# Optimization experiments

Hardware: AMD Instinct MI355X
Metric: run time of the kernel (lower is better)

The kernel has to match this reference:

```python
import jax, jax.numpy as jnp
import numpy as np

B, IN, H, G, WR = 8192, 1024, 1024, 2, 64
UR = [64, 64]


def setup_inputs() -> dict:
    key = jax.random.key(0)
    ks = jax.random.split(key, 9)
    hg = H // G
    return {
        "x": jax.random.normal(ks[0], (B, IN), jnp.float32),
        "h": jax.random.normal(ks[1], (B, H), jnp.float32),
        "c": jax.random.normal(ks[2], (B, H), jnp.float32),
        "u_x": 0.1 * jax.random.normal(ks[3], (IN, WR), jnp.float32),
        "v_x": 0.1 * jax.random.normal(ks[4], (4 * H, WR), jnp.float32),
        "u_h_0": 0.1 * jax.random.normal(ks[5], (G, hg, UR[0]), jnp.float32),
        "v_h_0": 0.1 * jax.random.normal(ks[6], (G, UR[0], 4 * hg), jnp.float32),
        "u_h_1": 0.1 * jax.random.normal(ks[7], (G, hg, UR[1]), jnp.float32),
        "v_h_1": 0.1 * jax.random.normal(ks[8], (G, UR[1], 4 * hg), jnp.float32),
        "bias_x": jnp.ones((1, 4 * H), jnp.float32),
        "bias_h": jnp.ones((1, 4 * H), jnp.float32),
    }


def reference(x, h, c, u_x, v_x, u_h_0, v_h_0, u_h_1, v_h_1, bias_x, bias_h):
    b = h.shape[0]
    hg = H // G
    # input-to-hidden low-rank projection: [B, 4H]
    gx = (x @ u_x) @ v_x.T + bias_x
    xf, xi, xn, xo = jnp.split(gx, 4, axis=1)  # each [B, H]

    hv = h.reshape(b, G, hg)  # [B, G, H/G]
    u_hs = [u_h_0, u_h_1]
    v_hs = [v_h_0, v_h_1]
    acc = None
    for i in range(G):
        # torch code rotates the group index list cumulatively each step:
        # step i uses permutation roll(arange(G), -i)
        perm = np.roll(np.arange(G), -i)
        h_op = hv[:, perm, :]  # [B, G, hg]
        t = jnp.einsum('bgd,gdr->bgr', h_op, u_hs[i])  # [B, G, r_i]
        t = jnp.einsum('bgr,grk->bgk', t, v_hs[i])     # [B, G, 4hg]
        acc = t if acc is None else acc + t

    # chunk along last dim into 4 gates, flatten group dim -> [B, H]
    f_h, i_h, n_h, o_h = [p.reshape(b, H) for p in jnp.split(acc, 4, axis=2)]
    hf, hi, hn, ho = jnp.split(bias_h, 4, axis=1)

    inputgate = jax.nn.sigmoid(xi + hi + i_h)
    forgetgate = jax.nn.sigmoid(xf + hf + f_h)
    outputgate = jax.nn.sigmoid(xo + ho + o_h)
    newgate = jnp.tanh(xn + hn + n_h)
    c_next = forgetgate * c + inputgate * newgate
    h_next = outputgate * jnp.tanh(c_next)
    return (h_next, c_next)
```

## Files before the change

kernel.cpp:

```cpp
#include <hip/hip_runtime.h>
#include <hip/hip_bf16.h>


typedef __bf16 bf16_t;
typedef __bf16 bf16x8 __attribute__((ext_vector_type(8)));
typedef float f32x4 __attribute__((ext_vector_type(4)));

#define MFMA16x16x32(a, b, c) __builtin_amdgcn_mfma_f32_16x16x32_bf16((a), (b), (c), 0, 0, 0)

#define T_OFF 0
#define UXT_OFF 5242880
#define UHT_OFF 5373952
#define WB_OFF 5636096

__global__ __launch_bounds__(256) void prep_kernel(
    const float* __restrict__ u_x, const float* __restrict__ u_h_0,
    const float* __restrict__ u_h_1, const float* __restrict__ v_h_0,
    const float* __restrict__ v_h_1, const float* __restrict__ v_x,
    bf16_t* __restrict__ uxT, bf16_t* __restrict__ uhT,
    bf16_t* __restrict__ Wb) {
  int i = blockIdx.x * 256 + threadIdx.x;
  if (i < 65536) {
    int j = i >> 10, k = i & 1023;
    uxT[i] = (bf16_t)u_x[k * 64 + j];
  } else if (i < 65536 + 131072) {
    int i2 = i - 65536;
    int s = i2 >> 15, rem = i2 & 32767;
    int j = rem >> 9, d = rem & 511;
    const float* src = (s & 1) ? u_h_1 : u_h_0;
    int goff = (s >> 1) ? 32768 : 0;
    uhT[i2] = (bf16_t)src[goff + d * 64 + j];
  } else if (i < 65536 + 131072 + 786432) {
    int e = i - 196608;
    int k = e % 192;
    int row = e / 192;
    int tile = row >> 7;
    int rr = row & 127;
    int g = tile >> 4, qt = tile & 15;
    int w = rr >> 5, ql = rr & 31;
    int m = g * 512 + qt * 32 + ql;
    int q = qt * 32 + ql;
    float val;
    if (k < 64)
      val = v_x[(w * 1024 + m) * 64 + k];
    else if (k < 128)
      val = v_h_0[g * 131072 + (k - 64) * 2048 + w * 512 + q];
    else
      val = v_h_1[g * 131072 + (k - 128) * 2048 + w * 512 + q];
    Wb[e] = (bf16_t)val;
  }
}

__global__ __launch_bounds__(256, 2) void phase1_kernel(
    const float* __restrict__ x, const float* __restrict__ h,
    const bf16_t* __restrict__ uxT, const bf16_t* __restrict__ uhT,
    bf16_t* __restrict__ T) {
  __shared__ bf16_t z[16][1048];
  const int b0 = blockIdx.x * 16;
  const int tid = threadIdx.x;
  const int wv = tid >> 6, lane = tid & 63;
  const int lo = lane & 15, quad = lane >> 4;
  const int srow = tid >> 4, sc = tid & 15;

  {
    const float* src = x + (size_t)(b0 + srow) * 1024;
#pragma unroll
    for (int j = 0; j < 16; ++j) {
      int col = sc * 4 + j * 64;
      float4 v = *(const float4*)(src + col);
      bf16_t* d = &z[srow][col];
      d[0] = (bf16_t)v.x; d[1] = (bf16_t)v.y;
      d[2] = (bf16_t)v.z; d[3] = (bf16_t)v.w;
    }
  }
  __syncthreads();

  f32x4 accx = {0.f, 0.f, 0.f, 0.f};
  {
    const bf16_t* wBase = uxT + (size_t)(16 * wv + lo) * 1024;
    for (int k = 0; k < 1024; k += 32) {
      bf16x8 af = *(const bf16x8*)&z[lo][k + quad * 8];
      bf16x8 bfr = *(const bf16x8*)(wBase + k + quad * 8);
      accx = MFMA16x16x32(af, bfr, accx);
    }
  }
#pragma unroll
  for (int r = 0; r < 4; ++r)
    T[(size_t)(b0 + quad * 4 + r) * 320 + 16 * wv + lo] = (bf16_t)accx[r];
  __syncthreads();

  {
    const float* src = h + (size_t)(b0 + srow) * 1024;
#pragma unroll
    for (int j = 0; j < 16; ++j) {
      int col = sc * 4 + j * 64;
      float4 v = *(const float4*)(src + col);
      bf16_t* d = &z[srow][col];
      d[0] = (bf16_t)v.x; d[1] = (bf16_t)v.y;
      d[2] = (bf16_t)v.z; d[3] = (bf16_t)v.w;
    }
  }
  __syncthreads();

  const int hoff = (wv == 1 || wv == 2) ? 512 : 0;
#pragma unroll
  for (int sub = 0; sub < 4; ++sub) {
    const bf16_t* wBase = uhT + (size_t)(wv * 64 + 16 * sub + lo) * 512;
    f32x4 acc = {0.f, 0.f, 0.f, 0.f};
    for (int k = 0; k < 512; k += 32) {
      bf16x8 af = *(const bf16x8*)&z[lo][hoff + k + quad * 8];
      bf16x8 bfr = *(const bf16x8*)(wBase + k + quad * 8);
      acc = MFMA16x16x32(af, bfr, acc);
    }
    int n = 64 + wv * 64 + sub * 16 + lo;
#pragma unroll
    for (int r = 0; r < 4; ++r)
      T[(size_t)(b0 + quad * 4 + r) * 320 + n] = (bf16_t)acc[r];
  }
}

__global__ __launch_bounds__(256, 3) void phase2_kernel(
    const bf16_t* __restrict__ T, const bf16_t* __restrict__ Wb,
    const float* __restrict__ bias_x, const float* __restrict__ bias_h,
    const float* __restrict__ c, float* __restrict__ out) {
  __shared__ bf16_t bs[128][200];

  const int b0 = blockIdx.x * 128;
  const int gq = blockIdx.y;
  const int g = gq >> 4, qt = gq & 15;
  const int tid = threadIdx.x;
  const int wv = tid >> 6, lane = tid & 63;
  const int lo = lane & 15, quad = lane >> 4;

  {
    const bf16_t* src = Wb + (size_t)gq * (128 * 192);
#pragma unroll
    for (int cch = 0; cch < 12; ++cch) {
      int lc = cch * 256 + tid;
      int row = lc / 24, col = (lc % 24) * 8;
      bf16x8 v = *(const bf16x8*)(src + (size_t)lc * 8);
      *(bf16x8*)&bs[row][col] = v;
    }
  }

  const int arow = b0 + wv * 32 + lo;
  bf16x8 a[2][6];
#pragma unroll
  for (int mt = 0; mt < 2; ++mt) {
    const bf16_t* tr = T + (size_t)(arow + mt * 16) * 320;
#pragma unroll
    for (int ks = 0; ks < 6; ++ks) {
      int col = (ks < 2) ? (ks * 32 + quad * 8)
                         : (64 + g * 128 + (ks - 2) * 32 + quad * 8);
      a[mt][ks] = *(const bf16x8*)(tr + col);
    }
  }
  __syncthreads();

  f32x4 acc[2][8];
#pragma unroll
  for (int mt = 0; mt < 2; ++mt)
#pragma unroll
    for (int nt = 0; nt < 8; ++nt) acc[mt][nt] = (f32x4){0.f, 0.f, 0.f, 0.f};

#pragma unroll
  for (int nt = 0; nt < 8; ++nt) {
#pragma unroll
    for (int ks = 0; ks < 6; ++ks) {
      bf16x8 bfr = *(const bf16x8*)&bs[nt * 16 + lo][ks * 32 + quad * 8];
      acc[0][nt] = MFMA16x16x32(a[0][ks], bfr, acc[0][nt]);
      acc[1][nt] = MFMA16x16x32(a[1][ks], bfr, acc[1][nt]);
    }
  }

  float bsum[4][2];
#pragma unroll
  for (int w = 0; w < 4; ++w)
#pragma unroll
    for (int cq = 0; cq < 2; ++cq) {
      int m = g * 512 + qt * 32 + cq * 16 + lo;
      int n = w * 1024 + m;
      bsum[w][cq] = bias_x[n] + bias_h[n];
    }

#pragma unroll
  for (int mt = 0; mt < 2; ++mt)
#pragma unroll
    for (int r = 0; r < 4; ++r) {
      int b = b0 + wv * 32 + mt * 16 + quad * 4 + r;
#pragma unroll
      for (int cq = 0; cq < 2; ++cq) {
        int m = g * 512 + qt * 32 + cq * 16 + lo;
        float fv = acc[mt][0 + cq][r] + bsum[0][cq];
        float iv = acc[mt][2 + cq][r] + bsum[1][cq];
        float nv = acc[mt][4 + cq][r] + bsum[2][cq];
        float ov = acc[mt][6 + cq][r] + bsum[3][cq];
        float cin = c[(size_t)b * 1024 + m];
        float ig = 1.f / (1.f + __expf(-iv));
        float fg = 1.f / (1.f + __expf(-fv));
        float og = 1.f / (1.f + __expf(-ov));
        float ng = tanhf(nv);
        float cn = fg * cin + ig * ng;
        float hn = og * tanhf(cn);
        out[(size_t)b * 1024 + m] = hn;
        out[8388608ull + (size_t)b * 1024 + m] = cn;
      }
    }
}

extern "C" void kernel_launch(void* const* d_in, const int* in_sizes, int n_in,
                              void* d_out, int out_size, void* d_ws,
                              size_t ws_size, hipStream_t stream) {
  const float* x = (const float*)d_in[0];
  const float* h = (const float*)d_in[1];
  const float* c = (const float*)d_in[2];
  const float* u_x = (const float*)d_in[3];
  const float* v_x = (const float*)d_in[4];
  const float* u_h_0 = (const float*)d_in[5];
  const float* v_h_0 = (const float*)d_in[6];
  const float* u_h_1 = (const float*)d_in[7];
  const float* v_h_1 = (const float*)d_in[8];
  const float* bias_x = (const float*)d_in[9];
  const float* bias_h = (const float*)d_in[10];

  char* ws = (char*)d_ws;
  bf16_t* T = (bf16_t*)(ws + T_OFF);
  bf16_t* uxT = (bf16_t*)(ws + UXT_OFF);
  bf16_t* uhT = (bf16_t*)(ws + UHT_OFF);
  bf16_t* Wb = (bf16_t*)(ws + WB_OFF);

  prep_kernel<<<3840, 256, 0, stream>>>(u_x, u_h_0, u_h_1, v_h_0, v_h_1, v_x,
                                        uxT, uhT, Wb);
  phase1_kernel<<<512, 256, 0, stream>>>(x, h, uxT, uhT, T);
  phase2_kernel<<<dim3(64, 32), 256, 0, stream>>>(T, Wb, bias_x, bias_h, c,
                                                  (float*)d_out);
}
```

Baseline: 233.1 us.

## Store weights and intermediates in MFMA fragment-native layouts; drop phase2 LDS staging

Prep now writes the U and W weights pre-swizzled into per-lane MFMA fragment order. Phase1 stages its outputs in LDS and writes the intermediate T in the same fragment-tiled layout, so phase2 can load A and B fragments with contiguous 16-byte per-lane global reads. This removes phase2's shared-memory tile, its staging loop and its barrier. It also restructures the phase1 h loop to reuse the A fragment across four subtiles, packs the bf16 converts into vector stores, and swaps in rcp-based sigmoid and tanh. Phase2 now reads B fragments straight from global memory through the cache, and the fast tanh may lose a little accuracy.

Measured after the change: 205.9 us. 11.7% less time.

```diff
diff --git a/kernel.cpp b/kernel.cpp
--- a/kernel.cpp
+++ b/kernel.cpp
@@ -3,41 +3,55 @@
 
 
 typedef __bf16 bf16_t;
+typedef __bf16 bf16x4 __attribute__((ext_vector_type(4)));
 typedef __bf16 bf16x8 __attribute__((ext_vector_type(8)));
 typedef float f32x4 __attribute__((ext_vector_type(4)));
 
 #define MFMA16x16x32(a, b, c) __builtin_amdgcn_mfma_f32_16x16x32_bf16((a), (b), (c), 0, 0, 0)
 
-#define T_OFF 0
-#define UXT_OFF 5242880
-#define UHT_OFF 5373952
-#define WB_OFF 5636096
+#define TA_OFF 0
+#define BX_OFF 5242880
+#define BH_OFF 5373952
+#define BW_OFF 5636096
+
+__device__ inline float fast_sigmoid(float x) {
+  return __builtin_amdgcn_rcpf(1.f + __expf(-x));
+}
+__device__ inline float fast_tanh(float x) {
+  return 2.f * __builtin_amdgcn_rcpf(1.f + __expf(-2.f * x)) - 1.f;
+}
 
 __global__ __launch_bounds__(256) void prep_kernel(
     const float* __restrict__ u_x, const float* __restrict__ u_h_0,
     const float* __restrict__ u_h_1, const float* __restrict__ v_h_0,
     const float* __restrict__ v_h_1, const float* __restrict__ v_x,
-    bf16_t* __restrict__ uxT, bf16_t* __restrict__ uhT,
-    bf16_t* __restrict__ Wb) {
-  int i = blockIdx.x * 256 + threadIdx.x;
-  if (i < 65536) {
-    int j = i >> 10, k = i & 1023;
-    uxT[i] = (bf16_t)u_x[k * 64 + j];
-  } else if (i < 65536 + 131072) {
-    int i2 = i - 65536;
-    int s = i2 >> 15, rem = i2 & 32767;
-    int j = rem >> 9, d = rem & 511;
+    bf16_t* __restrict__ Bx, bf16_t* __restrict__ Bh,
+    bf16_t* __restrict__ Bw) {
+  int o = blockIdx.x * 256 + threadIdx.x;
+  if (o < 65536) {
+    int j = o & 7, lane = (o >> 3) & 63, kk = (o >> 9) & 31, t = o >> 14;
+    int lo = lane & 15, quad = lane >> 4;
+    int k = kk * 32 + quad * 8 + j;
+    Bx[o] = (bf16_t)u_x[k * 64 + 16 * t + lo];
+  } else if (o < 196608) {
+    int o2 = o - 65536;
+    int j = o2 & 7, lane = (o2 >> 3) & 63, kk = (o2 >> 9) & 15;
+    int sub = (o2 >> 13) & 3, s = o2 >> 15;
+    int lo = lane & 15, quad = lane >> 4;
+    int d = kk * 32 + quad * 8 + j;
     const float* src = (s & 1) ? u_h_1 : u_h_0;
-    int goff = (s >> 1) ? 32768 : 0;
-    uhT[i2] = (bf16_t)src[goff + d * 64 + j];
-  } else if (i < 65536 + 131072 + 786432) {
-    int e = i - 196608;
-    int k = e % 192;
-    int row = e / 192;
-    int tile = row >> 7;
-    int rr = row & 127;
-    int g = tile >> 4, qt = tile & 15;
-    int w = rr >> 5, ql = rr & 31;
+    Bh[o2] = (bf16_t)src[(s >> 1) * 32768 + d * 64 + 16 * sub + lo];
+  } else if (o < 983040) {
+    int o3 = o - 196608;
+    int j = o3 & 7, lane = (o3 >> 3) & 63;
+    int chunk = o3 >> 9;
+    int ks = chunk % 6, rowt = chunk / 6;
+    int gq = rowt >> 3, nt = rowt & 7;
+    int lo = lane & 15, quad = lane >> 4;
+    int g = gq >> 4, qt = gq & 15;
+    int row = 16 * nt + lo;
+    int w = row >> 5, ql = row & 31;
+    int k = ks * 32 + quad * 8 + j;
     int m = g * 512 + qt * 32 + ql;
     int q = qt * 32 + ql;
     float val;
@@ -47,15 +61,16 @@
       val = v_h_0[g * 131072 + (k - 64) * 2048 + w * 512 + q];
     else
       val = v_h_1[g * 131072 + (k - 128) * 2048 + w * 512 + q];
-    Wb[e] = (bf16_t)val;
-  }
-}
-
-__global__ __launch_bounds__(256, 2) void phase1_kernel(
+    Bw[o3] = (bf16_t)val;
+  }
+}
+
+__global__ __launch_bounds__(256) void phase1_kernel(
     const float* __restrict__ x, const float* __restrict__ h,
-    const bf16_t* __restrict__ uxT, const bf16_t* __restrict__ uhT,
-    bf16_t* __restrict__ T) {
+    const bf16_t* __restrict__ Bx, const bf16_t* __restrict__ Bh,
+    bf16_t* __restrict__ TA) {
   __shared__ bf16_t z[16][1048];
+  __shared__ bf16_t pre[16][328];
   const int b0 = blockIdx.x * 16;
   const int tid = threadIdx.x;
   const int wv = tid >> 6, lane = tid & 63;
@@ -68,25 +83,25 @@
     for (int j = 0; j < 16; ++j) {
       int col = sc * 4 + j * 64;
       float4 v = *(const float4*)(src + col);
-      bf16_t* d = &z[srow][col];
-      d[0] = (bf16_t)v.x; d[1] = (bf16_t)v.y;
-      d[2] = (bf16_t)v.z; d[3] = (bf16_t)v.w;
-    }
-  }
-  __syncthreads();
-
-  f32x4 accx = {0.f, 0.f, 0.f, 0.f};
-  {
-    const bf16_t* wBase = uxT + (size_t)(16 * wv + lo) * 1024;
-    for (int k = 0; k < 1024; k += 32) {
-      bf16x8 af = *(const bf16x8*)&z[lo][k + quad * 8];
-      bf16x8 bfr = *(const bf16x8*)(wBase + k + quad * 8);
+      bf16x4 pk;
+      pk[0] = (bf16_t)v.x; pk[1] = (bf16_t)v.y;
+      pk[2] = (bf16_t)v.z; pk[3] = (bf16_t)v.w;
+      *(bf16x4*)&z[srow][col] = pk;
+    }
+  }
+  __syncthreads();
+
+  {
+    f32x4 accx = {0.f, 0.f, 0.f, 0.f};
+    const bf16_t* bx = Bx + ((size_t)(wv * 32) * 64 + lane) * 8;
+    for (int kk = 0; kk < 32; ++kk) {
+      bf16x8 af = *(const bf16x8*)&z[lo][kk * 32 + quad * 8];
+      bf16x8 bfr = *(const bf16x8*)(bx + (size_t)kk * 512);
       accx = MFMA16x16x32(af, bfr, accx);
     }
-  }
-#pragma unroll
-  for (int r = 0; r < 4; ++r)
-    T[(size_t)(b0 + quad * 4 + r) * 320 + 16 * wv + lo] = (bf16_t)accx[r];
+#pragma unroll
+    for (int r = 0; r < 4; ++r) pre[quad * 4 + r][16 * wv + lo] = (bf16_t)accx[r];
+  }
   __syncthreads();
 
   {
@@ -95,36 +110,53 @@
     for (int j = 0; j < 16; ++j) {
       int col = sc * 4 + j * 64;
       float4 v = *(const float4*)(src + col);
-      bf16_t* d = &z[srow][col];
-      d[0] = (bf16_t)v.x; d[1] = (bf16_t)v.y;
-      d[2] = (bf16_t)v.z; d[3] = (bf16_t)v.w;
-    }
-  }
-  __syncthreads();
-
-  const int hoff = (wv == 1 || wv == 2) ? 512 : 0;
-#pragma unroll
-  for (int sub = 0; sub < 4; ++sub) {
-    const bf16_t* wBase = uhT + (size_t)(wv * 64 + 16 * sub + lo) * 512;
-    f32x4 acc = {0.f, 0.f, 0.f, 0.f};
-    for (int k = 0; k < 512; k += 32) {
-      bf16x8 af = *(const bf16x8*)&z[lo][hoff + k + quad * 8];
-      bf16x8 bfr = *(const bf16x8*)(wBase + k + quad * 8);
-      acc = MFMA16x16x32(af, bfr, acc);
-    }
-    int n = 64 + wv * 64 + sub * 16 + lo;
-#pragma unroll
-    for (int r = 0; r < 4; ++r)
-      T[(size_t)(b0 + quad * 4 + r) * 320 + n] = (bf16_t)acc[r];
+      bf16x4 pk;
+      pk[0] = (bf16_t)v.x; pk[1] = (bf16_t)v.y;
+      pk[2] = (bf16_t)v.z; pk[3] = (bf16_t)v.w;
+      *(bf16x4*)&z[srow][col] = pk;
+    }
+  }
+  __syncthreads();
+
+  {
+    const int hoff = (wv == 1 || wv == 2) ? 512 : 0;
+    f32x4 acc[4];
+#pragma unroll
+    for (int sub = 0; sub < 4; ++sub) acc[sub] = (f32x4){0.f, 0.f, 0.f, 0.f};
+    for (int kk = 0; kk < 16; ++kk) {
+      bf16x8 af = *(const bf16x8*)&z[lo][hoff + kk * 32 + quad * 8];
+#pragma unroll
+      for (int sub = 0; sub < 4; ++sub) {
+        bf16x8 bfr = *(const bf16x8*)(Bh +
+            (((size_t)(wv * 4 + sub) * 16 + kk) * 64 + lane) * 8);
+        acc[sub] = MFMA16x16x32(af, bfr, acc[sub]);
+      }
+    }
+#pragma unroll
+    for (int sub = 0; sub < 4; ++sub) {
+      int n = 64 + wv * 64 + sub * 16 + lo;
+#pragma unroll
+      for (int r = 0; r < 4; ++r) pre[quad * 4 + r][n] = (bf16_t)acc[sub][r];
+    }
+  }
+  __syncthreads();
+
+#pragma unroll
+  for (int it = 0; it < 3; ++it) {
+    int slot = it * 256 + tid;
+    if (slot < 640) {
+      int cc = slot >> 6, ln = slot & 63;
+      int llo = ln & 15, lq = ln >> 4;
+      bf16x8 v = *(const bf16x8*)&pre[llo][cc * 32 + lq * 8];
+      *(bf16x8*)(TA + (((size_t)blockIdx.x * 10 + cc) * 64 + ln) * 8) = v;
+    }
   }
 }
 
 __global__ __launch_bounds__(256, 3) void phase2_kernel(
-    const bf16_t* __restrict__ T, const bf16_t* __restrict__ Wb,
+    const bf16_t* __restrict__ TA, const bf16_t* __restrict__ Bw,
     const float* __restrict__ bias_x, const float* __restrict__ bias_h,
     const float* __restrict__ c, float* __restrict__ out) {
-  __shared__ bf16_t bs[128][200];
-
   const int b0 = blockIdx.x * 128;
   const int gq = blockIdx.y;
   const int g = gq >> 4, qt = gq & 15;
@@ -132,30 +164,25 @@
   const int wv = tid >> 6, lane = tid & 63;
   const int lo = lane & 15, quad = lane >> 4;
 
-  {
-    const bf16_t* src = Wb + (size_t)gq * (128 * 192);
-#pragma unroll
-    for (int cch = 0; cch < 12; ++cch) {
-      int lc = cch * 256 + tid;
-      int row = lc / 24, col = (lc % 24) * 8;
-      bf16x8 v = *(const bf16x8*)(src + (size_t)lc * 8);
-      *(bf16x8*)&bs[row][col] = v;
-    }
-  }
-
-  const int arow = b0 + wv * 32 + lo;
   bf16x8 a[2][6];
 #pragma unroll
   for (int mt = 0; mt < 2; ++mt) {
-    const bf16_t* tr = T + (size_t)(arow + mt * 16) * 320;
+    int rt = blockIdx.x * 8 + wv * 2 + mt;
 #pragma unroll
     for (int ks = 0; ks < 6; ++ks) {
-      int col = (ks < 2) ? (ks * 32 + quad * 8)
-                         : (64 + g * 128 + (ks - 2) * 32 + quad * 8);
-      a[mt][ks] = *(const bf16x8*)(tr + col);
-    }
-  }
-  __syncthreads();
+      int cc = (ks < 2) ? ks : (g * 4 + ks);
+      a[mt][ks] = *(const bf16x8*)(TA + (((size_t)rt * 10 + cc) * 64 + lane) * 8);
+    }
+  }
+
+  float bsum[4][2];
+#pragma unroll
+  for (int w = 0; w < 4; ++w)
+#pragma unroll
+    for (int cq = 0; cq < 2; ++cq) {
+      int n = w * 1024 + g * 512 + qt * 32 + cq * 16 + lo;
+      bsum[w][cq] = bias_x[n] + bias_h[n];
+    }
 
   f32x4 acc[2][8];
 #pragma unroll
@@ -167,21 +194,12 @@
   for (int nt = 0; nt < 8; ++nt) {
 #pragma unroll
     for (int ks = 0; ks < 6; ++ks) {
-      bf16x8 bfr = *(const bf16x8*)&bs[nt * 16 + lo][ks * 32 + quad * 8];
+      bf16x8 bfr = *(const bf16x8*)(Bw +
+          (((size_t)(gq * 8 + nt) * 6 + ks) * 64 + lane) * 8);
       acc[0][nt] = MFMA16x16x32(a[0][ks], bfr, acc[0][nt]);
       acc[1][nt] = MFMA16x16x32(a[1][ks], bfr, acc[1][nt]);
     }
   }
-
-  float bsum[4][2];
-#pragma unroll
-  for (int w = 0; w < 4; ++w)
-#pragma unroll
-    for (int cq = 0; cq < 2; ++cq) {
-      int m = g * 512 + qt * 32 + cq * 16 + lo;
-      int n = w * 1024 + m;
-      bsum[w][cq] = bias_x[n] + bias_h[n];
-    }
 
 #pragma unroll
   for (int mt = 0; mt < 2; ++mt)
@@ -196,12 +214,12 @@
         float nv = acc[mt][4 + cq][r] + bsum[2][cq];
         float ov = acc[mt][6 + cq][r] + bsum[3][cq];
         float cin = c[(size_t)b * 1024 + m];
-        float ig = 1.f / (1.f + __expf(-iv));
-        float fg = 1.f / (1.f + __expf(-fv));
-        float og = 1.f / (1.f + __expf(-ov));
-        float ng = tanhf(nv);
+        float ig = fast_sigmoid(iv);
+        float fg = fast_sigmoid(fv);
+        float og = fast_sigmoid(ov);
+        float ng = fast_tanh(nv);
         float cn = fg * cin + ig * ng;
-        float hn = og * tanhf(cn);
+        float hn = og * fast_tanh(cn);
         out[(size_t)b * 1024 + m] = hn;
         out[8388608ull + (size_t)b * 1024 + m] = cn;
       }
@@ -224,14 +242,14 @@
   const float* bias_h = (const float*)d_in[10];
 
   char* ws = (char*)d_ws;
-  bf16_t* T = (bf16_t*)(ws + T_OFF);
-  bf16_t* uxT = (bf16_t*)(ws + UXT_OFF);
-  bf16_t* uhT = (bf16_t*)(ws + UHT_OFF);
-  bf16_t* Wb = (bf16_t*)(ws + WB_OFF);
+  bf16_t* TA = (bf16_t*)(ws + TA_OFF);
+  bf16_t* Bx = (bf16_t*)(ws + BX_OFF);
+  bf16_t* Bh = (bf16_t*)(ws + BH_OFF);
+  bf16_t* Bw = (bf16_t*)(ws + BW_OFF);
 
   prep_kernel<<<3840, 256, 0, stream>>>(u_x, u_h_0, u_h_1, v_h_0, v_h_1, v_x,
-                                        uxT, uhT, Wb);
-  phase1_kernel<<<512, 256, 0, stream>>>(x, h, uxT, uhT, T);
-  phase2_kernel<<<dim3(64, 32), 256, 0, stream>>>(T, Wb, bias_x, bias_h, c,
+                                        Bx, Bh, Bw);
+  phase1_kernel<<<512, 256, 0, stream>>>(x, h, Bx, Bh, TA);
+  phase2_kernel<<<dim3(64, 32), 256, 0, stream>>>(TA, Bw, bias_x, bias_h, c,
                                                   (float*)d_out);
 }
```
